# Kernel optimization log

Measured on AMD Instinct MI355X. Metric: run time of the kernel, lower is better.

## Reference

```python
import jax, jax.numpy as jnp
import numpy as np

HEADS = 8
DIM_HEAD = 64
NB_FEATURES = 256
DIM = 512

def setup_inputs() -> dict:
    key = jax.random.key(0)
    ks = jax.random.split(key, 4)
    b, n = 2, 8192
    x = jax.random.normal(ks[0], (b, n, DIM), jnp.float32)
    # fan-in scaling so exp(feature projections) stays numerically sane
    Wqkv = jax.random.normal(ks[1], (3 * HEADS * DIM_HEAD, DIM), jnp.float32) / np.sqrt(DIM).astype(np.float32)
    Wout = jax.random.normal(ks[2], (DIM, HEADS * DIM_HEAD), jnp.float32) / np.sqrt(HEADS * DIM_HEAD).astype(np.float32)
    bout = jnp.zeros((DIM,), jnp.float32)
    proj = jax.random.normal(ks[3], (NB_FEATURES, DIM_HEAD), jnp.float32) / np.sqrt(DIM_HEAD).astype(np.float32)
    return {"x": x, "Wqkv": Wqkv, "Wout": Wout, "bout": bout, "proj": proj}

def reference(x, Wqkv, Wout, bout, proj):
    b, n, _ = x.shape
    scale = DIM_HEAD ** -0.5
    qkv = jnp.einsum('bnd,ed->bne', x, Wqkv)            # [b,n,3*h*dh]
    q, k, v = jnp.split(qkv, 3, axis=-1)
    to_heads = lambda t: t.reshape(b, n, HEADS, DIM_HEAD).transpose(0, 2, 1, 3)  # [b,h,n,dh]
    q = to_heads(q) * scale
    k = to_heads(k)
    v = to_heads(v)
    # FAVOR+ exp feature maps
    q_prime = jnp.exp(jnp.einsum('bhnd,fd->bhnf', q, proj))  # [b,h,n,f]
    k_prime = jnp.exp(jnp.einsum('bhnd,fd->bhnf', k, proj))  # [b,h,n,f]
    k_sum = k_prime.sum(axis=2)                              # [b,h,f]
    D = jnp.einsum('bhnf,bhf->bhn', q_prime, k_sum)          # normalizer
    D_inv = 1.0 / (D + 1e-6)
    context = jnp.einsum('bhmf,bhmd->bhfd', k_prime, v)      # [b,h,f,dh]
    out = jnp.einsum('bhnf,bhfd->bhnd', q_prime, context) * D_inv[..., None]
    out = out.transpose(0, 2, 1, 3).reshape(b, n, HEADS * DIM_HEAD)
    return jnp.einsum('bne,de->bnd', out, Wout) + bout
```

## Files before the change

kernel.cpp:

```cpp
#include <hip/hip_runtime.h>
#include <math.h>

#define B_    2
#define NSEQ  8192
#define DIM_  512
#define H_    8
#define DH_   64
#define F_    256
#define M_    (B_*NSEQ)
#define QKV_  1536

typedef __attribute__((ext_vector_type(8))) short     short8;
typedef __attribute__((ext_vector_type(4))) float     float4v;
typedef __attribute__((ext_vector_type(8))) unsigned short ushort8v;

__device__ __forceinline__ unsigned short f2bf(float f) {
    unsigned u = __float_as_uint(f);
    u += 0x7FFFu + ((u >> 16) & 1u);
    return (unsigned short)(u >> 16);
}
__device__ __forceinline__ float bf2f(unsigned short h) {
    unsigned u = ((unsigned)h) << 16;
    return __uint_as_float(u);
}
__device__ __forceinline__ unsigned pack2bf(float lo, float hi) {
    return __builtin_amdgcn_perm(__float_as_uint(hi), __float_as_uint(lo), 0x07060302);
}
__device__ __forceinline__ void glds16(const void* g, void* s) {
    __builtin_amdgcn_global_load_lds(
        (const __attribute__((address_space(1))) unsigned int*)g,
        (__attribute__((address_space(3))) unsigned int*)s, 16, 0, 0);
}

__global__ __launch_bounds__(256) void cvt_all(const float* __restrict__ x,
                                               const float* __restrict__ wqkv,
                                               const float* __restrict__ wout,
                                               const float* __restrict__ proj,
                                               unsigned short* __restrict__ xb,
                                               unsigned short* __restrict__ wqkvb,
                                               unsigned short* __restrict__ woutb,
                                               unsigned short* __restrict__ projb) {
    int bid = blockIdx.x;
    const float* in; unsigned short* out; int i;
    if (bid < 4096)      { in = x;    out = xb;    i = bid * 256 + threadIdx.x; }
    else if (bid < 4480) { in = wqkv; out = wqkvb; i = (bid - 4096) * 256 + threadIdx.x; }
    else if (bid < 4608) { in = wout; out = woutb; i = (bid - 4480) * 256 + threadIdx.x; }
    else                 { in = proj; out = projb; i = (bid - 4608) * 256 + threadIdx.x; }
    float4 a = ((const float4*)in)[2 * i];
    float4 b = ((const float4*)in)[2 * i + 1];
    ushort8v o;
    o[0] = f2bf(a.x); o[1] = f2bf(a.y); o[2] = f2bf(a.z); o[3] = f2bf(a.w);
    o[4] = f2bf(b.x); o[5] = f2bf(b.y); o[6] = f2bf(b.z); o[7] = f2bf(b.w);
    ((ushort8v*)out)[i] = o;
}

template<bool BF16OUT>
__global__ __launch_bounds__(256) void gemm_nt_pp(const unsigned short* __restrict__ A,
                                                  const unsigned short* __restrict__ Bm,
                                                  const float* __restrict__ bias,
                                                  void* __restrict__ Cout,
                                                  unsigned short* __restrict__ vTout,
                                                  int M, int N, int K) {
    __shared__ __align__(16) unsigned short As[2][128 * 32];
    __shared__ __align__(16) unsigned short Bs[2][128 * 32];
    const int t  = threadIdx.x;
    const int w  = t >> 6, l = t & 63;
    const int wm = w >> 1, wn = w & 1;
    const int lr = l & 15, lq = l >> 4;

    const int gx = gridDim.x;
    int flat = blockIdx.y * gx + blockIdx.x;
    int per  = (gx * gridDim.y) >> 3;
    int flat2 = (flat & 7) * per + (flat >> 3);
    const int m0 = (flat2 / gx) * 128, n0 = (flat2 % gx) * 128;

    float4v acc[4][4];
#pragma unroll
    for (int mi = 0; mi < 4; mi++)
#pragma unroll
        for (int ni = 0; ni < 4; ni++) acc[mi][ni] = (float4v){0.f, 0.f, 0.f, 0.f};

    auto stage = [&](int buf, int k0) {
#pragma unroll
        for (int i = 0; i < 2; i++) {
            int rb8 = w * 2 + i;
            int row = rb8 * 16 + lr;
            glds16(A + (size_t)(m0 + row) * K + k0 + lq * 8, &As[buf][rb8 * 512]);
            glds16(Bm + (size_t)(n0 + row) * K + k0 + lq * 8, &Bs[buf][rb8 * 512]);
        }
    };

    const int nk = K >> 5;
    stage(0, 0);
    __syncthreads();

    for (int k = 0; k < nk; k++) {
        const int cur = k & 1;
        if (k + 1 < nk) stage(cur ^ 1, (k + 1) << 5);

        short8 af[4], bfr[4];
#pragma unroll
        for (int mi = 0; mi < 4; mi++)
            af[mi] = *(const short8*)&As[cur][((wm * 4 + mi) * 64 + l) * 8];
#pragma unroll
        for (int ni = 0; ni < 4; ni++)
            bfr[ni] = *(const short8*)&Bs[cur][((wn * 4 + ni) * 64 + l) * 8];
#pragma unroll
        for (int mi = 0; mi < 4; mi++)
#pragma unroll
            for (int ni = 0; ni < 4; ni++)
                acc[mi][ni] = __builtin_amdgcn_mfma_f32_16x16x32_bf16(
                    af[mi], bfr[ni], acc[mi][ni], 0, 0, 0);

        if (k + 1 < nk) __syncthreads();
    }

    const int q = l >> 4, c = l & 15;
#pragma unroll
    for (int mi = 0; mi < 4; mi++) {
        int row0 = m0 + wm * 64 + mi * 16 + q * 4;
#pragma unroll
        for (int ni = 0; ni < 4; ni++) {
            int col = n0 + wn * 64 + ni * 16 + c;
            if (BF16OUT && vTout != nullptr && col >= 1024) {
                int cm = col - 1024;
                int h2 = cm >> 6, dh = cm & 63;
                int bq = row0 >> 13;
                size_t nn = (size_t)(row0 & 8191);
                unsigned short* dst = vTout + (((size_t)bq * 8 + h2) * 64 + dh) * NSEQ + nn;
                uint2 pv;
                pv.x = ((unsigned)f2bf(acc[mi][ni][1]) << 16) | f2bf(acc[mi][ni][0]);
                pv.y = ((unsigned)f2bf(acc[mi][ni][3]) << 16) | f2bf(acc[mi][ni][2]);
                *(uint2*)dst = pv;
            } else {
                float bv = bias ? bias[col] : 0.f;
#pragma unroll
                for (int r = 0; r < 4; r++) {
                    float v = acc[mi][ni][r] + bv;
                    if (BF16OUT) ((unsigned short*)Cout)[(size_t)(row0 + r) * N + col] = f2bf(v);
                    else         ((float*)Cout)[(size_t)(row0 + r) * N + col] = v;
                }
            }
        }
    }
}

__global__ __launch_bounds__(256) void ctx_fused_mfma(
    const unsigned short* __restrict__ qkvb,
    const unsigned short* __restrict__ projb,
    const unsigned short* __restrict__ vT,
    unsigned short* __restrict__ partial)
{
    __shared__ __align__(16) unsigned short PB[16 * 512];
    __shared__ __align__(16) unsigned short KB[8 * 512];
    __shared__ __align__(16) unsigned short VB[8 * 512];
    __shared__ __align__(16) unsigned short KPA[16 * 512];
    const int t = threadIdx.x, w = t >> 6, l = t & 63;
    const int lr = l & 15, lq = l >> 4;
    const int s = blockIdx.x, fh = blockIdx.y, z = blockIdx.z;
    const int b = z >> 3, h = z & 7;
    const int nchunk = s * 512;

    for (int idx = w; idx < 16; idx += 4) {
        int fblk = idx >> 1, kt = idx & 1;
        glds16(projb + (size_t)(fh * 128 + fblk * 16 + lr) * 64 + kt * 32 + lq * 8, &PB[idx * 512]);
    }

    float4v acc[2][5];
#pragma unroll
    for (int mi = 0; mi < 2; mi++)
#pragma unroll
        for (int ni = 0; ni < 5; ni++) acc[mi][ni] = (float4v){0.f, 0.f, 0.f, 0.f};
    short ov = (lr == 0) ? (short)0x3F80 : (short)0;
    short8 ones = {ov, ov, ov, ov, ov, ov, ov, ov};

    for (int st = 0; st < 8; st++) {
        int nbase = nchunk + st * 64;
        __syncthreads();
        for (int idx = w; idx < 8; idx += 4) {
            int nblk = idx >> 1, kt = idx & 1;
            glds16(qkvb + ((size_t)b * NSEQ + nbase + nblk * 16 + lr) * QKV_ + 512 + h * 64 + kt * 32 + lq * 8,
                   &KB[idx * 512]);
        }
        for (int idx = w; idx < 8; idx += 4) {
            int dhb = idx >> 1, nt2 = idx & 1;
            glds16(vT + ((size_t)z * 64 + dhb * 16 + lr) * NSEQ + nbase + nt2 * 32 + lq * 8,
                   &VB[idx * 512]);
        }
        __syncthreads();

        float4v a2[4][2];
#pragma unroll
        for (int mi = 0; mi < 4; mi++)
#pragma unroll
            for (int ni = 0; ni < 2; ni++) a2[mi][ni] = (float4v){0.f, 0.f, 0.f, 0.f};
#pragma unroll
        for (int ks = 0; ks < 2; ks++) {
            short8 ka[4], pb[2];
#pragma unroll
            for (int mi = 0; mi < 4; mi++)
                ka[mi] = *(const short8*)&KB[((mi * 2 + ks) * 64 + l) * 8];
#pragma unroll
            for (int ni = 0; ni < 2; ni++)
                pb[ni] = *(const short8*)&PB[(((w * 2 + ni) * 2 + ks) * 64 + l) * 8];
#pragma unroll
            for (int mi = 0; mi < 4; mi++)
#pragma unroll
                for (int ni = 0; ni < 2; ni++)
                    a2[mi][ni] = __builtin_amdgcn_mfma_f32_16x16x32_bf16(ka[mi], pb[ni], a2[mi][ni], 0, 0, 0);
        }
#pragma unroll
        for (int mi = 0; mi < 4; mi++) {
            int nb = mi * 16 + lq * 4;
            int qoff = ((nb >> 3) & 3) * 256 + (nb & 7) * 2;
            int setn = nb >> 5;
#pragma unroll
            for (int ni = 0; ni < 2; ni++) {
                int fp = w * 32 + ni * 16 + lr;
                float e0 = __expf(a2[mi][ni][0]);
                float e1 = __expf(a2[mi][ni][1]);
                float e2 = __expf(a2[mi][ni][2]);
                float e3 = __expf(a2[mi][ni][3]);
                uint2 p; p.x = pack2bf(e0, e1); p.y = pack2bf(e2, e3);
                *(uint2*)((char*)KPA + (size_t)(((fp >> 4) * 2 + setn) * 1024 + qoff + (fp & 15) * 16)) = p;
            }
        }
#pragma unroll
        for (int ks = 0; ks < 2; ks++) {
            short8 af[2], bf[4];
#pragma unroll
            for (int mi = 0; mi < 2; mi++)
                af[mi] = *(const short8*)&KPA[(((w * 2 + mi) * 2 + ks) * 64 + l) * 8];
#pragma unroll
            for (int ni = 0; ni < 4; ni++)
                bf[ni] = *(const short8*)&VB[((ni * 2 + ks) * 64 + l) * 8];
#pragma unroll
            for (int mi = 0; mi < 2; mi++) {
#pragma unroll
                for (int ni = 0; ni < 4; ni++)
                    acc[mi][ni] = __builtin_amdgcn_mfma_f32_16x16x32_bf16(af[mi], bf[ni], acc[mi][ni], 0, 0, 0);
                acc[mi][4] = __builtin_amdgcn_mfma_f32_16x16x32_bf16(af[mi], ones, acc[mi][4], 0, 0, 0);
            }
        }
    }
    unsigned short* base = partial + (size_t)(s * 16 + z) * 80 * 256 + fh * 128;
#pragma unroll
    for (int mi = 0; mi < 2; mi++) {
        int f0r = w * 32 + mi * 16 + lq * 4;
#pragma unroll
        for (int ni = 0; ni < 5; ni++) {
            int col = ni * 16 + lr;
#pragma unroll
            for (int r = 0; r < 4; r++)
                base[(size_t)col * 256 + f0r + r] = f2bf(acc[mi][ni][r]);
        }
    }
}

__global__ __launch_bounds__(256) void ctx_reduce(const unsigned short* __restrict__ partial,
                                                  unsigned short* __restrict__ ctxT) {
    int idx8 = blockIdx.x * 256 + threadIdx.x;
    const int INNER = 16 * 80 * 256;
    size_t off = (size_t)idx8 * 8;
    float s0 = 0.f, s1 = 0.f, s2 = 0.f, s3 = 0.f, s4 = 0.f, s5 = 0.f, s6 = 0.f, s7 = 0.f;
#pragma unroll
    for (int k = 0; k < 16; k++) {
        ushort8v v = *(const ushort8v*)(partial + (size_t)k * INNER + off);
        s0 += bf2f(v[0]); s1 += bf2f(v[1]); s2 += bf2f(v[2]); s3 += bf2f(v[3]);
        s4 += bf2f(v[4]); s5 += bf2f(v[5]); s6 += bf2f(v[6]); s7 += bf2f(v[7]);
    }
    ushort8v o;
    o[0] = f2bf(s0); o[1] = f2bf(s1); o[2] = f2bf(s2); o[3] = f2bf(s3);
    o[4] = f2bf(s4); o[5] = f2bf(s5); o[6] = f2bf(s6); o[7] = f2bf(s7);
    *(ushort8v*)(ctxT + off) = o;
}

__global__ __launch_bounds__(256) void attn_fused_mfma(
    const unsigned short* __restrict__ qkvb,
    const unsigned short* __restrict__ projb,
    const unsigned short* __restrict__ ctxT,
    unsigned short* __restrict__ attnb)
{
    __shared__ __align__(16) unsigned short QB[16 * 512];
    __shared__ __align__(16) unsigned short PA[8 * 512];
    __shared__ __align__(16) unsigned short QPA[16 * 512];
    __shared__ __align__(16) unsigned short CB[10 * 512];
    const int t = threadIdx.x, w = t >> 6, l = t & 63;
    const int lr = l & 15, lq = l >> 4;
    const int m0 = blockIdx.x * 128, z = blockIdx.y;
    const int b = z >> 3, h = z & 7;

    for (int idx = w; idx < 16; idx += 4) {
        int mblk = idx >> 1, kt = idx & 1;
        glds16(qkvb + ((size_t)b * NSEQ + m0 + mblk * 16 + lr) * QKV_ + h * 64 + kt * 32 + lq * 8,
               &QB[idx * 512]);
    }
    float4v acc[2][5];
#pragma unroll
    for (int mi = 0; mi < 2; mi++)
#pragma unroll
        for (int ni = 0; ni < 5; ni++) acc[mi][ni] = (float4v){0.f, 0.f, 0.f, 0.f};

    for (int fs = 0; fs < 4; fs++) {
        int f0 = fs * 64;
        __syncthreads();
        for (int idx = w; idx < 8; idx += 4) {
            int fb = idx >> 1, kt = idx & 1;
            glds16(projb + (size_t)(f0 + fb * 16 + lr) * 64 + kt * 32 + lq * 8, &PA[idx * 512]);
        }
        for (int idx = w; idx < 10; idx += 4) {
            int dhb = idx >> 1, ft = idx & 1;
            glds16(ctxT + ((size_t)z * 80 + dhb * 16 + lr) * 256 + f0 + ft * 32 + lq * 8,
                   &CB[idx * 512]);
        }
        __syncthreads();

        float4v a2[4][2];
#pragma unroll
        for (int mi = 0; mi < 4; mi++)
#pragma unroll
            for (int ni = 0; ni < 2; ni++) a2[mi][ni] = (float4v){0.f, 0.f, 0.f, 0.f};
#pragma unroll
        for (int ks = 0; ks < 2; ks++) {
            short8 pa[4], qb[2];
#pragma unroll
            for (int mi = 0; mi < 4; mi++)
                pa[mi] = *(const short8*)&PA[((mi * 2 + ks) * 64 + l) * 8];
#pragma unroll
            for (int ni = 0; ni < 2; ni++)
                qb[ni] = *(const short8*)&QB[(((w * 2 + ni) * 2 + ks) * 64 + l) * 8];
#pragma unroll
            for (int mi = 0; mi < 4; mi++)
#pragma unroll
                for (int ni = 0; ni < 2; ni++)
                    a2[mi][ni] = __builtin_amdgcn_mfma_f32_16x16x32_bf16(pa[mi], qb[ni], a2[mi][ni], 0, 0, 0);
        }
#pragma unroll
        for (int mi = 0; mi < 4; mi++) {
            int fb2 = mi * 16 + lq * 4;
            int qoff = ((fb2 >> 3) & 3) * 256 + (fb2 & 7) * 2;
            int setf = fb2 >> 5;
#pragma unroll
            for (int ni = 0; ni < 2; ni++) {
                int m = w * 32 + ni * 16 + lr;
                float e0 = __expf(0.125f * a2[mi][ni][0]);
                float e1 = __expf(0.125f * a2[mi][ni][1]);
                float e2 = __expf(0.125f * a2[mi][ni][2]);
                float e3 = __expf(0.125f * a2[mi][ni][3]);
                uint2 p; p.x = pack2bf(e0, e1); p.y = pack2bf(e2, e3);
                *(uint2*)((char*)QPA + (size_t)(((m >> 4) * 2 + setf) * 1024 + qoff + (m & 15) * 16)) = p;
            }
        }
#pragma unroll
        for (int ks = 0; ks < 2; ks++) {
            short8 af[2], cb[5];
#pragma unroll
            for (int mi = 0; mi < 2; mi++)
                af[mi] = *(const short8*)&QPA[(((w * 2 + mi) * 2 + ks) * 64 + l) * 8];
#pragma unroll
            for (int ni = 0; ni < 5; ni++)
                cb[ni] = *(const short8*)&CB[((ni * 2 + ks) * 64 + l) * 8];
#pragma unroll
            for (int mi = 0; mi < 2; mi++)
#pragma unroll
                for (int ni = 0; ni < 5; ni++)
                    acc[mi][ni] = __builtin_amdgcn_mfma_f32_16x16x32_bf16(af[mi], cb[ni], acc[mi][ni], 0, 0, 0);
        }
    }
#pragma unroll
    for (int mi = 0; mi < 2; mi++) {
        int rowb = m0 + w * 32 + mi * 16 + lq * 4;
#pragma unroll
        for (int r = 0; r < 4; r++) {
            float dv = __shfl(acc[mi][4][r], (l & 48), 64);
            float rinv = 1.f / (dv + 1e-6f);
#pragma unroll
            for (int ni = 0; ni < 4; ni++)
                attnb[((size_t)b * NSEQ + rowb + r) * 512 + h * 64 + ni * 16 + lr] =
                    f2bf(acc[mi][ni][r] * rinv);
        }
    }
}

extern "C" void kernel_launch(void* const* d_in, const int* in_sizes, int n_in,
                              void* d_out, int out_size, void* d_ws, size_t ws_size,
                              hipStream_t stream) {
    const float* x    = (const float*)d_in[0];
    const float* Wqkv = (const float*)d_in[1];
    const float* Wout = (const float*)d_in[2];
    const float* bout = (const float*)d_in[3];
    const float* proj = (const float*)d_in[4];

    unsigned short* qkvb    = (unsigned short*)d_ws;
    unsigned short* vT      = qkvb + (size_t)M_ * QKV_;
    unsigned short* partial = vT + (size_t)16 * 64 * NSEQ;
    unsigned short* ctxT    = partial + (size_t)16 * 16 * 80 * 256;
    unsigned short* projb   = ctxT + (size_t)16 * 80 * 256;
    unsigned short* xb      = projb + 16384;
    unsigned short* attnb   = xb;
    unsigned short* wqkvb   = xb + (size_t)M_ * DIM_;
    unsigned short* woutb   = wqkvb + (size_t)QKV_ * DIM_;
    float* outp = (float*)d_out;

    cvt_all<<<dim3(4616), 256, 0, stream>>>(x, Wqkv, Wout, proj, xb, wqkvb, woutb, projb);
    gemm_nt_pp<true><<<dim3(QKV_ / 128, M_ / 128), 256, 0, stream>>>(xb, wqkvb, nullptr, qkvb, vT, M_, QKV_, DIM_);
    ctx_fused_mfma<<<dim3(16, 2, 16), 256, 0, stream>>>(qkvb, projb, vT, partial);
    ctx_reduce<<<dim3(160), 256, 0, stream>>>(partial, ctxT);
    attn_fused_mfma<<<dim3(64, 16), 256, 0, stream>>>(qkvb, projb, ctxT, attnb);
    gemm_nt_pp<false><<<dim3(DIM_ / 128, M_ / 128), 256, 0, stream>>>(attnb, woutb, bout, outp, nullptr, M_, DIM_, DIM_);
}
```

Baseline: 212.5 us.

## Enlarge GEMM tiles to 256x128 with triple-buffered BK=64 pipeline

The bf16 NT GEMM used for the QKV and output projections now runs 512 threads per block over a 256x128 output tile. It uses a K-step of 64, and its LDS staging is triple-buffered. Explicit vmcnt waits plus raw barriers replace the per-iteration __syncthreads, so loads for two stages ahead stay in flight while MFMAs run, and the MFMA section is given raised wave priority. The aim is to cut barrier overhead and memory latency stalls and to reuse each B tile across more rows. In exchange, LDS use grows to about 144KB per block, which limits occupancy, and the K loop is hardcoded to 8 iterations, assuming K=512.

```diff
diff --git a/kernel.cpp b/kernel.cpp
--- a/kernel.cpp
+++ b/kernel.cpp
@@ -55,14 +55,14 @@
 }
 
 template<bool BF16OUT>
-__global__ __launch_bounds__(256) void gemm_nt_pp(const unsigned short* __restrict__ A,
+__global__ __launch_bounds__(512) void gemm_nt_pp(const unsigned short* __restrict__ A,
                                                   const unsigned short* __restrict__ Bm,
                                                   const float* __restrict__ bias,
                                                   void* __restrict__ Cout,
                                                   unsigned short* __restrict__ vTout,
                                                   int M, int N, int K) {
-    __shared__ __align__(16) unsigned short As[2][128 * 32];
-    __shared__ __align__(16) unsigned short Bs[2][128 * 32];
+    __shared__ __align__(16) unsigned short As[3][32 * 512];
+    __shared__ __align__(16) unsigned short Bs[3][16 * 512];
     const int t  = threadIdx.x;
     const int w  = t >> 6, l = t & 63;
     const int wm = w >> 1, wn = w & 1;
@@ -72,7 +72,7 @@
     int flat = blockIdx.y * gx + blockIdx.x;
     int per  = (gx * gridDim.y) >> 3;
     int flat2 = (flat & 7) * per + (flat >> 3);
-    const int m0 = (flat2 / gx) * 128, n0 = (flat2 % gx) * 128;
+    const int m0 = (flat2 / gx) * 256, n0 = (flat2 % gx) * 128;
 
     float4v acc[4][4];
 #pragma unroll
@@ -82,37 +82,52 @@
 
     auto stage = [&](int buf, int k0) {
 #pragma unroll
+        for (int i = 0; i < 4; i++) {
+            int c = w * 4 + i, rb = c >> 1, ks = c & 1;
+            glds16(A + (size_t)(m0 + rb * 16 + lr) * K + k0 + ks * 32 + lq * 8,
+                   &As[buf][c * 512]);
+        }
+#pragma unroll
         for (int i = 0; i < 2; i++) {
-            int rb8 = w * 2 + i;
-            int row = rb8 * 16 + lr;
-            glds16(A + (size_t)(m0 + row) * K + k0 + lq * 8, &As[buf][rb8 * 512]);
-            glds16(Bm + (size_t)(n0 + row) * K + k0 + lq * 8, &Bs[buf][rb8 * 512]);
+            int c = w * 2 + i, rb = c >> 1, ks = c & 1;
+            glds16(Bm + (size_t)(n0 + rb * 16 + lr) * K + k0 + ks * 32 + lq * 8,
+                   &Bs[buf][c * 512]);
         }
     };
 
-    const int nk = K >> 5;
     stage(0, 0);
-    __syncthreads();
-
-    for (int k = 0; k < nk; k++) {
-        const int cur = k & 1;
-        if (k + 1 < nk) stage(cur ^ 1, (k + 1) << 5);
-
-        short8 af[4], bfr[4];
-#pragma unroll
-        for (int mi = 0; mi < 4; mi++)
-            af[mi] = *(const short8*)&As[cur][((wm * 4 + mi) * 64 + l) * 8];
-#pragma unroll
-        for (int ni = 0; ni < 4; ni++)
-            bfr[ni] = *(const short8*)&Bs[cur][((wn * 4 + ni) * 64 + l) * 8];
-#pragma unroll
-        for (int mi = 0; mi < 4; mi++)
+    stage(1, 64);
+
+#pragma unroll
+    for (int k = 0; k < 8; k++) {
+        if (k < 7) { asm volatile("s_waitcnt vmcnt(6)" ::: "memory"); }
+        else       { asm volatile("s_waitcnt vmcnt(0)" ::: "memory"); }
+        __builtin_amdgcn_s_barrier();
+        const int cur = k % 3;
+
+        if (k + 2 < 8) stage((k + 2) % 3, (k + 2) << 6);
+
+        short8 af[2][4], bfr[2][4];
+#pragma unroll
+        for (int ks = 0; ks < 2; ks++) {
+#pragma unroll
+            for (int mi = 0; mi < 4; mi++)
+                af[ks][mi] = *(const short8*)&As[cur][(((wm * 4 + mi) * 2 + ks) * 64 + l) * 8];
 #pragma unroll
             for (int ni = 0; ni < 4; ni++)
-                acc[mi][ni] = __builtin_amdgcn_mfma_f32_16x16x32_bf16(
-                    af[mi], bfr[ni], acc[mi][ni], 0, 0, 0);
-
-        if (k + 1 < nk) __syncthreads();
+                bfr[ks][ni] = *(const short8*)&Bs[cur][(((wn * 4 + ni) * 2 + ks) * 64 + l) * 8];
+        }
+
+        __builtin_amdgcn_s_setprio(1);
+#pragma unroll
+        for (int ks = 0; ks < 2; ks++)
+#pragma unroll
+            for (int mi = 0; mi < 4; mi++)
+#pragma unroll
+                for (int ni = 0; ni < 4; ni++)
+                    acc[mi][ni] = __builtin_amdgcn_mfma_f32_16x16x32_bf16(
+                        af[ks][mi], bfr[ks][ni], acc[mi][ni], 0, 0, 0);
+        __builtin_amdgcn_s_setprio(0);
     }
 
     const int q = l >> 4, c = l & 15;
@@ -403,9 +418,9 @@
     float* outp = (float*)d_out;
 
     cvt_all<<<dim3(4616), 256, 0, stream>>>(x, Wqkv, Wout, proj, xb, wqkvb, woutb, projb);
-    gemm_nt_pp<true><<<dim3(QKV_ / 128, M_ / 128), 256, 0, stream>>>(xb, wqkvb, nullptr, qkvb, vT, M_, QKV_, DIM_);
+    gemm_nt_pp<true><<<dim3(QKV_ / 128, M_ / 256), 512, 0, stream>>>(xb, wqkvb, nullptr, qkvb, vT, M_, QKV_, DIM_);
     ctx_fused_mfma<<<dim3(16, 2, 16), 256, 0, stream>>>(qkvb, projb, vT, partial);
     ctx_reduce<<<dim3(160), 256, 0, stream>>>(partial, ctxT);
     attn_fused_mfma<<<dim3(64, 16), 256, 0, stream>>>(qkvb, projb, ctxT, attnb);
-    gemm_nt_pp<false><<<dim3(DIM_ / 128, M_ / 128), 256, 0, stream>>>(attnb, woutb, bout, outp, nullptr, M_, DIM_, DIM_);
-}
+    gemm_nt_pp<false><<<dim3(DIM_ / 128, M_ / 256), 512, 0, stream>>>(attnb, woutb, bout, outp, nullptr, M_, DIM_, DIM_);
+}
```

After: 208.4 us. No clear change (-1.9%).
